# Kernel tuning notes

Measured on AMD Instinct MI355X. Metric: run time of the kernel, lower is better.

The kernel has to match this reference:

```python
import jax, jax.numpy as jnp
import numpy as np

SIGMA = 10.0   # init kwarg sigma
NODE_IDX = 28  # teeth per arch
P = 320        # points per tooth
D = 3


def setup_inputs() -> dict:
    key = jax.random.key(0)
    k1, k2 = jax.random.split(key)
    X_v = jax.random.normal(k1, (NODE_IDX, P, D), dtype=jnp.float32)
    target_X_v = jax.random.normal(k2, (NODE_IDX, P, D), dtype=jnp.float32)
    return {"X_v": X_v, "target_X_v": target_X_v, "node_idx": NODE_IDX}


def _chamfer_sum(x, y):
    # x: [N,3], y: [M,3]. Squared-L2 chamfer with point_reduction='sum' both
    # directions and batch_reduction='sum' (batch size 1) as in pytorch3d.
    d = (jnp.sum(x * x, axis=-1)[:, None]
         + jnp.sum(y * y, axis=-1)[None, :]
         - 2.0 * (x @ y.T))  # [N, M] squared distances
    return jnp.min(d, axis=1).sum() + jnp.min(d, axis=0).sum()


def _gather_idx(node_idx):
    # Per-node subset: drop node idx, append paired node (idx+mid or idx-mid).
    mid = (node_idx - 2) // 2
    rows = []
    for idx in range(node_idx - 2):
        extra = idx + mid if idx < mid else idx - mid
        rows.append([j for j in range(node_idx) if j != idx] + [extra])
    return np.asarray(rows, dtype=np.int32), mid


def reference(X_v, target_X_v, node_idx):
    n, p, d = X_v.shape
    cX = jnp.clip(X_v, -SIGMA, SIGMA)
    cT = jnp.clip(target_X_v, -SIGMA, SIGMA)
    idx_mat, mid = _gather_idx(node_idx)           # [node_idx-2, node_idx]
    subs_x = cX[idx_mat].reshape(node_idx - 2, n * p, d)
    subs_t = cT[idx_mat].reshape(node_idx - 2, n * p, d)

    def body(acc, xt):
        x, t = xt
        return acc + _chamfer_sum(x, t), None

    loss, _ = jax.lax.scan(body, jnp.float32(0.0), (subs_x, subs_t))
    # idx == node_idx-2: first half of the arch; idx == node_idx-1: second half
    loss = loss + _chamfer_sum(cX[:mid].reshape(-1, d), cT[:mid].reshape(-1, d))
    loss = loss + _chamfer_sum(cX[mid:].reshape(-1, d), cT[mid:].reshape(-1, d))
    return loss
```

## Files before the change

kernel.cpp:

```cpp
#include <hip/hip_runtime.h>

#define NODES  28
#define PPN    320
#define MID    13
#define NPTS   (NODES * PPN)
#define TOTPTS (2 * NPTS)
#define SIGMA  10.0f
#define FLT_BIG 3.4e38f

#define BT    128
#define RPT   2
#define GPTS  (BT * RPT)
#define NGRP  (NPTS / GPTS)

__global__ __launch_bounds__(BT)
void pair_min_kernel(const float* __restrict__ X, const float* __restrict__ T,
                     float* __restrict__ m)
{
    __shared__ float4 st[PPN];

    const int bid = blockIdx.x;
    const int p   = bid / (NGRP * NODES);
    const int r   = bid % (NGRP * NODES);
    const int g   = r / NODES;
    const int b   = r % NODES;

    const float* __restrict__ src = p ? T : X;
    const float* __restrict__ db  = p ? X : T;

    const int t = threadIdx.x;

    for (int j = t; j < PPN; j += BT) {
        const float* q = db + (size_t)(b * PPN + j) * 3;
        float v0 = fminf(fmaxf(q[0], -SIGMA), SIGMA);
        float v1 = fminf(fmaxf(q[1], -SIGMA), SIGMA);
        float v2 = fminf(fmaxf(q[2], -SIGMA), SIGMA);
        float n  = v0*v0 + v1*v1 + v2*v2;
        st[j] = make_float4(-2.f*v0, -2.f*v1, -2.f*v2, n);
    }

    const int i0 = g * GPTS + t;
    const int i1 = i0 + BT;
    float4 s0, s1;
    {
        const float* q0 = src + (size_t)i0 * 3;
        float a0 = fminf(fmaxf(q0[0], -SIGMA), SIGMA);
        float a1 = fminf(fmaxf(q0[1], -SIGMA), SIGMA);
        float a2 = fminf(fmaxf(q0[2], -SIGMA), SIGMA);
        s0 = make_float4(a0, a1, a2, a0*a0 + a1*a1 + a2*a2);
        const float* q1 = src + (size_t)i1 * 3;
        float b0 = fminf(fmaxf(q1[0], -SIGMA), SIGMA);
        float b1 = fminf(fmaxf(q1[1], -SIGMA), SIGMA);
        float b2 = fminf(fmaxf(q1[2], -SIGMA), SIGMA);
        s1 = make_float4(b0, b1, b2, b0*b0 + b1*b1 + b2*b2);
    }
    __syncthreads();

    float mn0 = FLT_BIG, mn1 = FLT_BIG;
    #pragma unroll 4
    for (int j = 0; j < PPN; j += 2) {
        const float4 ta = st[j];
        const float4 tb = st[j + 1];
        float d0a = fmaf(ta.x, s0.x, fmaf(ta.y, s0.y, fmaf(ta.z, s0.z, ta.w)));
        float d0b = fmaf(tb.x, s0.x, fmaf(tb.y, s0.y, fmaf(tb.z, s0.z, tb.w)));
        float d1a = fmaf(ta.x, s1.x, fmaf(ta.y, s1.y, fmaf(ta.z, s1.z, ta.w)));
        float d1b = fmaf(tb.x, s1.x, fmaf(tb.y, s1.y, fmaf(tb.z, s1.z, tb.w)));
        mn0 = fminf(mn0, fminf(d0a, d0b));
        mn1 = fminf(mn1, fminf(d1a, d1b));
    }

    const int q0 = p * NPTS + i0;
    float* row = m + (size_t)b * TOTPTS;
    row[q0]      = mn0 + s0.w;
    row[q0 + BT] = mn1 + s1.w;
}

__inline__ __device__ float wave_reduce_sum(float v) {
    #pragma unroll
    for (int off = 32; off > 0; off >>= 1)
        v += __shfl_down(v, off, 64);
    return v;
}

__global__ __launch_bounds__(256)
void combine_kernel(const float* __restrict__ m,
                    float* __restrict__ out)
{
    const int q = blockIdx.x * blockDim.x + threadIdx.x;
    float tot = 0.0f;
    if (q < TOTPTS) {
        const int a = (q % NPTS) / PPN;

        float r[NODES];
        #pragma unroll
        for (int c = 0; c < NODES; ++c) r[c] = m[(size_t)c * TOTPTS + q];

        float min1 = FLT_BIG; int c1 = -1;
        #pragma unroll
        for (int c = 0; c < NODES; ++c) {
            if (r[c] < min1) { min1 = r[c]; c1 = c; }
        }
        float min2 = FLT_BIG;
        #pragma unroll
        for (int c = 0; c < NODES; ++c) {
            float v = (c == c1) ? FLT_BIG : r[c];
            min2 = fminf(min2, v);
        }
        float H = FLT_BIG;
        if (a < MID) {
            #pragma unroll
            for (int c = 0; c < MID; ++c) H = fminf(H, r[c]);
        } else {
            #pragma unroll
            for (int c = MID; c < NODES; ++c) H = fminf(H, r[c]);
        }

        const int n = (a < NODES - 2) ? (NODES - 3) : (NODES - 2);
        float S = (float)n * min1;
        if (c1 <= NODES - 3 && c1 != a) S -= (min1 - min2);
        if (a < NODES - 2) {
            const int dup = (a < MID) ? (a + MID) : (a - MID);
            S += (c1 == dup) ? min2 : min1;
        }
        tot = S + H;
    }

    __shared__ float warp_sums[4];
    float ws = wave_reduce_sum(tot);
    const int lane = threadIdx.x & 63;
    const int wid  = threadIdx.x >> 6;
    if (lane == 0) warp_sums[wid] = ws;
    __syncthreads();
    if (wid == 0) {
        float v = (lane < 4) ? warp_sums[lane] : 0.0f;
        v = wave_reduce_sum(v);
        if (lane == 0) atomicAdd(out, v);
    }
}

extern "C" void kernel_launch(void* const* d_in, const int* in_sizes, int n_in,
                              void* d_out, int out_size, void* d_ws, size_t ws_size,
                              hipStream_t stream) {
    const float* X = (const float*)d_in[0];
    const float* T = (const float*)d_in[1];
    float* out = (float*)d_out;
    float* m   = (float*)d_ws;

    hipMemsetAsync(out, 0, sizeof(float), stream);
    pair_min_kernel<<<2 * NGRP * NODES, BT, 0, stream>>>(X, T, m);
    combine_kernel<<<(TOTPTS + 255) / 256, 256, 0, stream>>>(m, out);
}
```

Baseline: 75.11 us.

## Register-block 10 query points per thread and split database tiles across blocks

Each thread now keeps 10 query points in registers instead of 2, so every shared-memory database point it loads is reused across more distance evaluations. The per-node database of 320 points is split into 4 slices of 80, each handled by its own block, to keep the grid large. Each slice writes its own partial minima, and the combine kernel now takes the minimum over the 4 slices before its existing logic. The cost is a 4x larger intermediate buffer and 4x more global reads in the combine step, plus smaller 64-thread blocks.

```diff
diff --git a/kernel.cpp b/kernel.cpp
--- a/kernel.cpp
+++ b/kernel.cpp
@@ -8,30 +8,34 @@
 #define SIGMA  10.0f
 #define FLT_BIG 3.4e38f
 
-#define BT    128
-#define RPT   2
+#define BT    64
+#define RPT   10
 #define GPTS  (BT * RPT)
 #define NGRP  (NPTS / GPTS)
+#define DBT   80
+#define NDBT  (PPN / DBT)
 
-__global__ __launch_bounds__(BT)
+__global__ __launch_bounds__(BT, 3)
 void pair_min_kernel(const float* __restrict__ X, const float* __restrict__ T,
                      float* __restrict__ m)
 {
-    __shared__ float4 st[PPN];
+    __shared__ float4 st[DBT];
 
     const int bid = blockIdx.x;
-    const int p   = bid / (NGRP * NODES);
-    const int r   = bid % (NGRP * NODES);
-    const int g   = r / NODES;
-    const int b   = r % NODES;
+    const int p   = bid / (NGRP * NODES * NDBT);
+    const int r1  = bid % (NGRP * NODES * NDBT);
+    const int g   = r1 / (NODES * NDBT);
+    const int r2  = r1 % (NODES * NDBT);
+    const int b   = r2 / NDBT;
+    const int s   = r2 % NDBT;
 
     const float* __restrict__ src = p ? T : X;
     const float* __restrict__ db  = p ? X : T;
 
     const int t = threadIdx.x;
 
-    for (int j = t; j < PPN; j += BT) {
-        const float* q = db + (size_t)(b * PPN + j) * 3;
+    for (int j = t; j < DBT; j += BT) {
+        const float* q = db + (size_t)(b * PPN + s * DBT + j) * 3;
         float v0 = fminf(fmaxf(q[0], -SIGMA), SIGMA);
         float v1 = fminf(fmaxf(q[1], -SIGMA), SIGMA);
         float v2 = fminf(fmaxf(q[2], -SIGMA), SIGMA);
@@ -39,40 +43,37 @@
         st[j] = make_float4(-2.f*v0, -2.f*v1, -2.f*v2, n);
     }
 
-    const int i0 = g * GPTS + t;
-    const int i1 = i0 + BT;
-    float4 s0, s1;
-    {
-        const float* q0 = src + (size_t)i0 * 3;
-        float a0 = fminf(fmaxf(q0[0], -SIGMA), SIGMA);
-        float a1 = fminf(fmaxf(q0[1], -SIGMA), SIGMA);
-        float a2 = fminf(fmaxf(q0[2], -SIGMA), SIGMA);
-        s0 = make_float4(a0, a1, a2, a0*a0 + a1*a1 + a2*a2);
-        const float* q1 = src + (size_t)i1 * 3;
-        float b0 = fminf(fmaxf(q1[0], -SIGMA), SIGMA);
-        float b1 = fminf(fmaxf(q1[1], -SIGMA), SIGMA);
-        float b2 = fminf(fmaxf(q1[2], -SIGMA), SIGMA);
-        s1 = make_float4(b0, b1, b2, b0*b0 + b1*b1 + b2*b2);
+    float4 sp[RPT];
+    #pragma unroll
+    for (int k = 0; k < RPT; ++k) {
+        const float* q = src + (size_t)(g * GPTS + k * BT + t) * 3;
+        float a0 = fminf(fmaxf(q[0], -SIGMA), SIGMA);
+        float a1 = fminf(fmaxf(q[1], -SIGMA), SIGMA);
+        float a2 = fminf(fmaxf(q[2], -SIGMA), SIGMA);
+        sp[k] = make_float4(a0, a1, a2, a0*a0 + a1*a1 + a2*a2);
     }
     __syncthreads();
 
-    float mn0 = FLT_BIG, mn1 = FLT_BIG;
-    #pragma unroll 4
-    for (int j = 0; j < PPN; j += 2) {
+    float mn[RPT];
+    #pragma unroll
+    for (int k = 0; k < RPT; ++k) mn[k] = FLT_BIG;
+
+    #pragma unroll 2
+    for (int j = 0; j < DBT; j += 2) {
         const float4 ta = st[j];
         const float4 tb = st[j + 1];
-        float d0a = fmaf(ta.x, s0.x, fmaf(ta.y, s0.y, fmaf(ta.z, s0.z, ta.w)));
-        float d0b = fmaf(tb.x, s0.x, fmaf(tb.y, s0.y, fmaf(tb.z, s0.z, tb.w)));
-        float d1a = fmaf(ta.x, s1.x, fmaf(ta.y, s1.y, fmaf(ta.z, s1.z, ta.w)));
-        float d1b = fmaf(tb.x, s1.x, fmaf(tb.y, s1.y, fmaf(tb.z, s1.z, tb.w)));
-        mn0 = fminf(mn0, fminf(d0a, d0b));
-        mn1 = fminf(mn1, fminf(d1a, d1b));
+        #pragma unroll
+        for (int k = 0; k < RPT; ++k) {
+            float da = fmaf(ta.x, sp[k].x, fmaf(ta.y, sp[k].y, fmaf(ta.z, sp[k].z, ta.w)));
+            float dbv = fmaf(tb.x, sp[k].x, fmaf(tb.y, sp[k].y, fmaf(tb.z, sp[k].z, tb.w)));
+            mn[k] = fminf(mn[k], fminf(da, dbv));
+        }
     }
 
-    const int q0 = p * NPTS + i0;
-    float* row = m + (size_t)b * TOTPTS;
-    row[q0]      = mn0 + s0.w;
-    row[q0 + BT] = mn1 + s1.w;
+    float* row = m + ((size_t)s * NODES + b) * TOTPTS + (p * NPTS + g * GPTS);
+    #pragma unroll
+    for (int k = 0; k < RPT; ++k)
+        row[k * BT + t] = mn[k] + sp[k].w;
 }
 
 __inline__ __device__ float wave_reduce_sum(float v) {
@@ -93,7 +94,13 @@
 
         float r[NODES];
         #pragma unroll
-        for (int c = 0; c < NODES; ++c) r[c] = m[(size_t)c * TOTPTS + q];
+        for (int c = 0; c < NODES; ++c) {
+            float v = m[(size_t)c * TOTPTS + q];
+            #pragma unroll
+            for (int s = 1; s < NDBT; ++s)
+                v = fminf(v, m[((size_t)s * NODES + c) * TOTPTS + q]);
+            r[c] = v;
+        }
 
         float min1 = FLT_BIG; int c1 = -1;
         #pragma unroll
@@ -147,6 +154,6 @@
     float* m   = (float*)d_ws;
 
     hipMemsetAsync(out, 0, sizeof(float), stream);
-    pair_min_kernel<<<2 * NGRP * NODES, BT, 0, stream>>>(X, T, m);
+    pair_min_kernel<<<2 * NGRP * NODES * NDBT, BT, 0, stream>>>(X, T, m);
     combine_kernel<<<(TOTPTS + 255) / 256, 256, 0, stream>>>(m, out);
 }
```

Measured after the change: 89.79 us. 1.2x slower.
